# Performance work log

Measured on AMD Instinct MI355X. Metric: run time of the kernel, lower is better.

## Reference

```python
import jax, jax.numpy as jnp
import numpy as np

MODEL_DIM = 1024
NUM_HEADS = 16
HEAD_DIM = MODEL_DIM // NUM_HEADS


def setup_inputs() -> dict:
    key = jax.random.key(0)
    ks = jax.random.split(key, 9)
    s = 1.0 / np.sqrt(MODEL_DIM)
    d = {
        "query": jax.random.normal(ks[0], (2, 2048, MODEL_DIM), dtype=jnp.float32),
        "Wq": jax.random.normal(ks[1], (MODEL_DIM, MODEL_DIM), dtype=jnp.float32) * s,
        "bq": jnp.zeros((MODEL_DIM,), dtype=jnp.float32),
        "Wk": jax.random.normal(ks[2], (MODEL_DIM, MODEL_DIM), dtype=jnp.float32) * s,
        "bk": jnp.zeros((MODEL_DIM,), dtype=jnp.float32),
        "Wv": jax.random.normal(ks[3], (MODEL_DIM, MODEL_DIM), dtype=jnp.float32) * s,
        "bv": jnp.zeros((MODEL_DIM,), dtype=jnp.float32),
        "Wo": jax.random.normal(ks[4], (MODEL_DIM, MODEL_DIM), dtype=jnp.float32) * s,
        "bo": jnp.zeros((MODEL_DIM,), dtype=jnp.float32),
    }
    return d


def reference(query, Wq, bq, Wk, bk, Wv, bv, Wo, bo):
    B, S, D = query.shape
    H, hd = NUM_HEADS, HEAD_DIM
    # self-attention: key = value = query
    q = (query @ Wq.T + bq).reshape(B, S, H, hd).transpose(0, 2, 1, 3)  # [B,H,S,hd]
    k = (query @ Wk.T + bk).reshape(B, S, H, hd).transpose(0, 2, 1, 3)
    v = (query @ Wv.T + bv).reshape(B, S, H, hd).transpose(0, 2, 1, 3)
    scores = jnp.einsum("bhqd,bhkd->bhqk", q, k) / np.sqrt(hd)  # [B,H,S,S]
    attn = jax.nn.softmax(scores, axis=-1)
    ctx = jnp.einsum("bhqk,bhkd->bhqd", attn, v)  # [B,H,S,hd]
    ctx = ctx.transpose(0, 2, 1, 3).reshape(B, S, D)
    return ctx @ Wo.T + bo
```

## Files before the change

### kernel.cpp

```cpp
#include <hip/hip_runtime.h>

typedef __attribute__((ext_vector_type(8))) __bf16 bf16x8;
typedef __attribute__((ext_vector_type(8))) unsigned short ushort8;
typedef __attribute__((ext_vector_type(4))) unsigned short ushort4v;
typedef __attribute__((ext_vector_type(4))) float f32x4;
typedef __attribute__((ext_vector_type(2))) _Float16 f16x2;
typedef __attribute__((ext_vector_type(4))) _Float16 f16x4;
typedef __attribute__((ext_vector_type(8))) _Float16 f16x8;
typedef __attribute__((ext_vector_type(2))) __fp16 fp16v2;

__device__ __forceinline__ unsigned short f2bf(float f) {
    union { float f; unsigned int u; } c; c.f = f;
    unsigned int u = c.u;
    u += 0x7fffu + ((u >> 16) & 1u);
    return (unsigned short)(u >> 16);
}

__device__ __forceinline__ void async16(const void* g, void* l) {
    __builtin_amdgcn_global_load_lds(
        (const __attribute__((address_space(1))) unsigned int*)g,
        (__attribute__((address_space(3))) unsigned int*)l, 16, 0, 0);
}

__global__ __launch_bounds__(256) void cvt_all(
    const float* __restrict__ q,  const float* __restrict__ wq,
    const float* __restrict__ wk, const float* __restrict__ wv,
    const float* __restrict__ wo,
    unsigned short* __restrict__ q_bf, unsigned short* __restrict__ wqkv,
    unsigned short* __restrict__ wo_bf, float scale_k)
{
    const int NQ = 4096 * 1024, NW = 1024 * 1024;
    int i = (blockIdx.x * 256 + threadIdx.x) * 4;
    const float* src; unsigned short* dst; float sc = 1.0f; int off;
    if (i < NQ)               { src = q;  dst = q_bf;          off = i; }
    else if (i < NQ + NW)     { src = wq; dst = wqkv;          off = i - NQ; }
    else if (i < NQ + 2 * NW) { src = wk; dst = wqkv + NW;     off = i - NQ - NW; sc = scale_k; }
    else if (i < NQ + 3 * NW) { src = wv; dst = wqkv + 2 * NW; off = i - NQ - 2 * NW; }
    else                      { src = wo; dst = wo_bf;         off = i - NQ - 3 * NW; }
    float4 v = *(const float4*)(src + off);
    ushort4v o;
    o[0] = f2bf(v.x * sc); o[1] = f2bf(v.y * sc);
    o[2] = f2bf(v.z * sc); o[3] = f2bf(v.w * sc);
    *(ushort4v*)(dst + off) = o;
}

__global__ __launch_bounds__(256) void qkv_gemm(
    const unsigned short* __restrict__ A,
    const unsigned short* __restrict__ B,
    unsigned short* __restrict__ Cout,
    const float* __restrict__ b0, const float* __restrict__ b1, const float* __restrict__ b2,
    float s1)
{
    __shared__ __align__(16) unsigned short As[128 * 64];
    __shared__ __align__(16) unsigned short Bs[128 * 64];

    const int tid  = threadIdx.x;
    const int lane = tid & 63, wave = tid >> 6;
    const int quad = lane >> 4, l15 = lane & 15;
    const int wm = wave >> 1, wn = wave & 1;
    const int by = blockIdx.y, bx = blockIdx.x;
    const int K = 1024, N = 3072;

    const int srow = lane >> 3;
    const int sp   = lane & 7;
    const int scl  = sp ^ srow;
    const int sw   = l15 & 7;

    f32x4 acc[4][4];
#pragma unroll
    for (int i = 0; i < 4; ++i)
#pragma unroll
        for (int j = 0; j < 4; ++j) acc[i][j] = (f32x4)(0.0f);

    for (int kt = 0; kt < 16; ++kt) {
        __syncthreads();
#pragma unroll
        for (int j = 0; j < 4; ++j) {
            int r0 = wave * 32 + j * 8;
            async16(A + (size_t)(by * 128 + r0 + srow) * K + kt * 64 + scl * 8, &As[r0 * 64]);
            async16(B + (size_t)(bx * 128 + r0 + srow) * K + kt * 64 + scl * 8, &Bs[r0 * 64]);
        }
        __syncthreads();

#pragma unroll
        for (int kh = 0; kh < 2; ++kh) {
            bf16x8 af[4], bfr[4];
#pragma unroll
            for (int mi = 0; mi < 4; ++mi)
                af[mi] = __builtin_bit_cast(bf16x8,
                    *(const ushort8*)&As[(wm * 64 + mi * 16 + l15) * 64 + ((kh * 4 + quad) ^ sw) * 8]);
#pragma unroll
            for (int ni = 0; ni < 4; ++ni)
                bfr[ni] = __builtin_bit_cast(bf16x8,
                    *(const ushort8*)&Bs[(wn * 64 + ni * 16 + l15) * 64 + ((kh * 4 + quad) ^ sw) * 8]);
#pragma unroll
            for (int mi = 0; mi < 4; ++mi)
#pragma unroll
                for (int ni = 0; ni < 4; ++ni)
                    acc[mi][ni] = __builtin_amdgcn_mfma_f32_16x16x32_bf16(af[mi], bfr[ni], acc[mi][ni], 0, 0, 0);
        }
    }

#pragma unroll
    for (int ni = 0; ni < 4; ++ni) {
        int n = bx * 128 + wn * 64 + ni * 16 + l15;
        float bias = (n < 1024) ? b0[n] : (n < 2048 ? b1[n - 1024] * s1 : b2[n - 2048]);
#pragma unroll
        for (int mi = 0; mi < 4; ++mi) {
#pragma unroll
            for (int r = 0; r < 4; ++r) {
                int m = by * 128 + wm * 64 + mi * 16 + quad * 4 + r;
                Cout[(size_t)m * N + n] = f2bf(acc[mi][ni][r] + bias);
            }
        }
    }
}

__global__ __launch_bounds__(256) void out_gemm(
    const unsigned short* __restrict__ A,
    const unsigned short* __restrict__ B,
    float* __restrict__ Cout,
    const float* __restrict__ bo)
{
    __shared__ __align__(16) unsigned short As[128 * 64];
    __shared__ __align__(16) unsigned short Bs[64 * 64];

    const int tid  = threadIdx.x;
    const int lane = tid & 63, wave = tid >> 6;
    const int quad = lane >> 4, l15 = lane & 15;
    const int wm = wave >> 1, wn = wave & 1;
    const int by = blockIdx.y, bx = blockIdx.x;
    const int K = 1024;

    const int srow = lane >> 3;
    const int sp   = lane & 7;
    const int scl  = sp ^ srow;
    const int sw   = l15 & 7;

    f32x4 acc[4][2];
#pragma unroll
    for (int i = 0; i < 4; ++i)
#pragma unroll
        for (int j = 0; j < 2; ++j) acc[i][j] = (f32x4)(0.0f);

    for (int kt = 0; kt < 16; ++kt) {
        __syncthreads();
#pragma unroll
        for (int j = 0; j < 4; ++j) {
            int r0 = wave * 32 + j * 8;
            async16(A + (size_t)(by * 128 + r0 + srow) * K + kt * 64 + scl * 8, &As[r0 * 64]);
        }
#pragma unroll
        for (int j = 0; j < 2; ++j) {
            int r0 = wave * 16 + j * 8;
            async16(B + (size_t)(bx * 64 + r0 + srow) * K + kt * 64 + scl * 8, &Bs[r0 * 64]);
        }
        __syncthreads();

#pragma unroll
        for (int kh = 0; kh < 2; ++kh) {
            bf16x8 af[4], bfr[2];
#pragma unroll
            for (int mi = 0; mi < 4; ++mi)
                af[mi] = __builtin_bit_cast(bf16x8,
                    *(const ushort8*)&As[(wm * 64 + mi * 16 + l15) * 64 + ((kh * 4 + quad) ^ sw) * 8]);
#pragma unroll
            for (int ni = 0; ni < 2; ++ni)
                bfr[ni] = __builtin_bit_cast(bf16x8,
                    *(const ushort8*)&Bs[(wn * 32 + ni * 16 + l15) * 64 + ((kh * 4 + quad) ^ sw) * 8]);
#pragma unroll
            for (int mi = 0; mi < 4; ++mi)
#pragma unroll
                for (int ni = 0; ni < 2; ++ni)
                    acc[mi][ni] = __builtin_amdgcn_mfma_f32_16x16x32_bf16(af[mi], bfr[ni], acc[mi][ni], 0, 0, 0);
        }
    }

#pragma unroll
    for (int ni = 0; ni < 2; ++ni) {
        int n = bx * 64 + wn * 32 + ni * 16 + l15;
        float bias = bo[n];
#pragma unroll
        for (int mi = 0; mi < 4; ++mi) {
#pragma unroll
            for (int r = 0; r < 4; ++r) {
                int m = by * 128 + wm * 64 + mi * 16 + quad * 4 + r;
                Cout[(size_t)m * 1024 + n] = acc[mi][ni][r] + bias;
            }
        }
    }
}

__global__ __launch_bounds__(256) void transpose_v(const unsigned short* __restrict__ qkv,
                                                   _Float16* __restrict__ vtg)
{
    __shared__ unsigned short Ls[64][68];
    const int tid = threadIdx.x;
    const int bh = blockIdx.y, st = blockIdx.x;
    const int b = bh >> 4, h = bh & 15;

#pragma unroll
    for (int i = 0; i < 2; ++i) {
        int s = tid + i * 256;
        int row = s >> 3, c8 = (s & 7) << 3;
        ushort8 v = *(const ushort8*)(qkv + (size_t)(b * 2048 + st * 64 + row) * 3072 + 2048 + h * 64 + c8);
        *(ushort8*)&Ls[row][c8] = v;
    }
    __syncthreads();
#pragma unroll
    for (int i = 0; i < 2; ++i) {
        int s = tid + i * 256;
        int hd = s >> 3, p = s & 7;
        int cl = p ^ (hd & 7);
        int g = cl >> 2, q = cl & 3;
        f16x8 o;
#pragma unroll
        for (int e = 0; e < 8; ++e) {
            int kv = g * 32 + (e >> 2) * 16 + q * 4 + (e & 3);
            union { float f; unsigned int u; } c;
            c.u = ((unsigned int)Ls[kv][hd]) << 16;
            o[e] = (_Float16)c.f;
        }
        *(f16x8*)(vtg + (size_t)(bh * 64 + hd) * 2048 + st * 64 + p * 8) = o;
    }
}

__global__ __launch_bounds__(256) void attn(const unsigned short* __restrict__ qkv,
                                            const _Float16* __restrict__ vtg,
                                            unsigned short* __restrict__ ctx)
{
    __shared__ __align__(16) unsigned short Ks[64 * 64];
    __shared__ __align__(16) _Float16 Vt[64 * 64];

    const int tid  = threadIdx.x;
    const int lane = tid & 63, wave = tid >> 6;
    const int quad = lane >> 4, l15 = lane & 15;
    const int bh = blockIdx.y;
    const int b = bh >> 4, h = bh & 15;
    const int q0 = blockIdx.x * 128;

    const int srow = lane >> 3;
    const int sp   = lane & 7;
    const int scl  = sp ^ srow;
    const int sw   = l15 & 7;

    bf16x8 qf[2][2];
#pragma unroll
    for (int s = 0; s < 2; ++s) {
        int qrow = b * 2048 + q0 + wave * 32 + s * 16 + l15;
#pragma unroll
        for (int kh = 0; kh < 2; ++kh)
            qf[s][kh] = __builtin_bit_cast(bf16x8,
                *(const ushort8*)(qkv + (size_t)qrow * 3072 + h * 64 + kh * 32 + quad * 8));
    }

    f32x4 ot[2][4];
#pragma unroll
    for (int s = 0; s < 2; ++s)
#pragma unroll
        for (int ht = 0; ht < 4; ++ht) ot[s][ht] = (f32x4)(0.0f);
    float l_acc[2] = {0.0f, 0.0f};
    const fp16v2 ones = {(__fp16)1.0f, (__fp16)1.0f};

    for (int kt = 0; kt < 32; ++kt) {
        __syncthreads();
#pragma unroll
        for (int i = 0; i < 2; ++i) {
            int row = i * 32 + wave * 8 + srow;
            async16(qkv + (size_t)(b * 2048 + kt * 64 + row) * 3072 + 1024 + h * 64 + scl * 8,
                    &Ks[(i * 32 + wave * 8) * 64]);
            async16(vtg + (size_t)(bh * 64 + row) * 2048 + kt * 64 + sp * 8,
                    (unsigned short*)&Vt[(i * 32 + wave * 8) * 64]);
        }
        __syncthreads();

        f16x4 pv[2][4];
#pragma unroll
        for (int mt = 0; mt < 4; ++mt) {
            const unsigned short* kb = &Ks[(mt * 16 + l15) * 64];
            bf16x8 k0 = __builtin_bit_cast(bf16x8, *(const ushort8*)(kb + (quad ^ sw) * 8));
            bf16x8 k1 = __builtin_bit_cast(bf16x8, *(const ushort8*)(kb + ((quad ^ sw) ^ 4) * 8));
#pragma unroll
            for (int s = 0; s < 2; ++s) {
                f32x4 s4 = (f32x4)(0.0f);
                s4 = __builtin_amdgcn_mfma_f32_16x16x32_bf16(k0, qf[s][0], s4, 0, 0, 0);
                s4 = __builtin_amdgcn_mfma_f32_16x16x32_bf16(k1, qf[s][1], s4, 0, 0, 0);
                float p0 = __builtin_amdgcn_exp2f(s4[0]);
                float p1 = __builtin_amdgcn_exp2f(s4[1]);
                float p2 = __builtin_amdgcn_exp2f(s4[2]);
                float p3 = __builtin_amdgcn_exp2f(s4[3]);
                fp16v2 lo = __builtin_amdgcn_cvt_pkrtz(p0, p1);
                fp16v2 hi = __builtin_amdgcn_cvt_pkrtz(p2, p3);
                l_acc[s] = __builtin_amdgcn_fdot2(lo, ones, l_acc[s], false);
                l_acc[s] = __builtin_amdgcn_fdot2(hi, ones, l_acc[s], false);
                f16x2 lo2 = __builtin_bit_cast(f16x2, lo);
                f16x2 hi2 = __builtin_bit_cast(f16x2, hi);
                pv[s][mt] = __builtin_shufflevector(lo2, hi2, 0, 1, 2, 3);
            }
        }

#pragma unroll
        for (int ht = 0; ht < 4; ++ht) {
            const _Float16* vb = &Vt[(ht * 16 + l15) * 64];
#pragma unroll
            for (int g = 0; g < 2; ++g) {
                f16x8 v8 = *(const f16x8*)(vb + (((g * 4 + quad) ^ sw)) * 8);
                f16x4 vlo = __builtin_shufflevector(v8, v8, 0, 1, 2, 3);
                f16x4 vhi = __builtin_shufflevector(v8, v8, 4, 5, 6, 7);
#pragma unroll
                for (int s = 0; s < 2; ++s) {
                    ot[s][ht] = __builtin_amdgcn_mfma_f32_16x16x16f16(vlo, pv[s][2 * g],     ot[s][ht], 0, 0, 0);
                    ot[s][ht] = __builtin_amdgcn_mfma_f32_16x16x16f16(vhi, pv[s][2 * g + 1], ot[s][ht], 0, 0, 0);
                }
            }
        }
    }

#pragma unroll
    for (int s = 0; s < 2; ++s) {
        float l = l_acc[s];
        l += __shfl_xor(l, 16, 64);
        l += __shfl_xor(l, 32, 64);
        float inv = 1.0f / l;
        int qrow = b * 2048 + q0 + wave * 32 + s * 16 + l15;
#pragma unroll
        for (int ht = 0; ht < 4; ++ht) {
            ushort4v o4;
#pragma unroll
            for (int r = 0; r < 4; ++r) o4[r] = f2bf(ot[s][ht][r] * inv);
            *(ushort4v*)(ctx + (size_t)qrow * 1024 + h * 64 + ht * 16 + quad * 4) = o4;
        }
    }
}

extern "C" void kernel_launch(void* const* d_in, const int* in_sizes, int n_in,
                              void* d_out, int out_size, void* d_ws, size_t ws_size,
                              hipStream_t stream) {
    const float* query = (const float*)d_in[0];
    const float* Wq = (const float*)d_in[1];
    const float* bq = (const float*)d_in[2];
    const float* Wk = (const float*)d_in[3];
    const float* bk = (const float*)d_in[4];
    const float* Wv = (const float*)d_in[5];
    const float* bv = (const float*)d_in[6];
    const float* Wo = (const float*)d_in[7];
    const float* bo = (const float*)d_in[8];

    char* ws = (char*)d_ws;
    unsigned short* q_bf  = (unsigned short*)(ws);
    _Float16*       vtg   = (_Float16*)(ws);
    unsigned short* wqkv  = (unsigned short*)(ws + 8388608);
    unsigned short* wo_bf = (unsigned short*)(ws + 14680064);
    unsigned short* qkv   = (unsigned short*)(ws + 16777216);
    unsigned short* ctx   = (unsigned short*)(ws + 41943040);

    const float SCALE = 0.125f * 1.4426950408889634f;

    cvt_all<<<8192, 256, 0, stream>>>(query, Wq, Wk, Wv, Wo, q_bf, wqkv, wo_bf, SCALE);
    qkv_gemm<<<dim3(24, 32), 256, 0, stream>>>(q_bf, wqkv, qkv, bq, bk, bv, SCALE);
    transpose_v<<<dim3(32, 32), 256, 0, stream>>>(qkv, vtg);
    attn<<<dim3(16, 32), 256, 0, stream>>>(qkv, vtg, ctx);
    out_gemm<<<dim3(16, 32), 256, 0, stream>>>(ctx, wo_bf, (float*)d_out, bo);
}
```

Measured before the change: 202.9 us.

## Double-buffer LDS tiles in output GEMM and attention kernels

Splits the shared-memory tiles of the output projection GEMM and the attention kernel into two buffers. The next K/V or A/B tile is issued with async global-to-LDS loads while the current buffer is being computed, with two barriers per pair of iterations. This is meant to hide global load latency that was previously exposed between the load and compute barriers. In exchange it doubles LDS usage per block, which may lower occupancy. If the compiler inserts conservative vmcnt waits before the LDS reads, the overlap may be lost.

Result: slower. 207.7 us (+2.4%).

```diff
diff --git a/kernel.cpp b/kernel.cpp
--- a/kernel.cpp
+++ b/kernel.cpp
@@ -122,8 +122,8 @@
     float* __restrict__ Cout,
     const float* __restrict__ bo)
 {
-    __shared__ __align__(16) unsigned short As[128 * 64];
-    __shared__ __align__(16) unsigned short Bs[64 * 64];
+    __shared__ __align__(16) unsigned short As[2][128 * 64];
+    __shared__ __align__(16) unsigned short Bs[2][64 * 64];
 
     const int tid  = threadIdx.x;
     const int lane = tid & 63, wave = tid >> 6;
@@ -143,37 +143,47 @@
 #pragma unroll
         for (int j = 0; j < 2; ++j) acc[i][j] = (f32x4)(0.0f);
 
-    for (int kt = 0; kt < 16; ++kt) {
-        __syncthreads();
+    auto stage = [&](int kt, int p) {
 #pragma unroll
         for (int j = 0; j < 4; ++j) {
             int r0 = wave * 32 + j * 8;
-            async16(A + (size_t)(by * 128 + r0 + srow) * K + kt * 64 + scl * 8, &As[r0 * 64]);
+            async16(A + (size_t)(by * 128 + r0 + srow) * K + kt * 64 + scl * 8, &As[p][r0 * 64]);
         }
 #pragma unroll
         for (int j = 0; j < 2; ++j) {
             int r0 = wave * 16 + j * 8;
-            async16(B + (size_t)(bx * 64 + r0 + srow) * K + kt * 64 + scl * 8, &Bs[r0 * 64]);
-        }
-        __syncthreads();
-
+            async16(B + (size_t)(bx * 64 + r0 + srow) * K + kt * 64 + scl * 8, &Bs[p][r0 * 64]);
+        }
+    };
+
+    auto compute = [&](int p) {
 #pragma unroll
         for (int kh = 0; kh < 2; ++kh) {
             bf16x8 af[4], bfr[2];
 #pragma unroll
             for (int mi = 0; mi < 4; ++mi)
                 af[mi] = __builtin_bit_cast(bf16x8,
-                    *(const ushort8*)&As[(wm * 64 + mi * 16 + l15) * 64 + ((kh * 4 + quad) ^ sw) * 8]);
+                    *(const ushort8*)&As[p][(wm * 64 + mi * 16 + l15) * 64 + ((kh * 4 + quad) ^ sw) * 8]);
 #pragma unroll
             for (int ni = 0; ni < 2; ++ni)
                 bfr[ni] = __builtin_bit_cast(bf16x8,
-                    *(const ushort8*)&Bs[(wn * 32 + ni * 16 + l15) * 64 + ((kh * 4 + quad) ^ sw) * 8]);
+                    *(const ushort8*)&Bs[p][(wn * 32 + ni * 16 + l15) * 64 + ((kh * 4 + quad) ^ sw) * 8]);
 #pragma unroll
             for (int mi = 0; mi < 4; ++mi)
 #pragma unroll
                 for (int ni = 0; ni < 2; ++ni)
                     acc[mi][ni] = __builtin_amdgcn_mfma_f32_16x16x32_bf16(af[mi], bfr[ni], acc[mi][ni], 0, 0, 0);
         }
+    };
+
+    stage(0, 0);
+    for (int t = 0; t < 8; ++t) {
+        __syncthreads();
+        stage(2 * t + 1, 1);
+        compute(0);
+        __syncthreads();
+        if (t < 7) stage(2 * t + 2, 0);
+        compute(1);
     }
 
 #pragma unroll
@@ -229,8 +239,8 @@
                                             const _Float16* __restrict__ vtg,
                                             unsigned short* __restrict__ ctx)
 {
-    __shared__ __align__(16) unsigned short Ks[64 * 64];
-    __shared__ __align__(16) _Float16 Vt[64 * 64];
+    __shared__ __align__(16) unsigned short Ks[2][64 * 64];
+    __shared__ __align__(16) _Float16 Vt[2][64 * 64];
 
     const int tid  = threadIdx.x;
     const int lane = tid & 63, wave = tid >> 6;
@@ -244,6 +254,19 @@
     const int scl  = sp ^ srow;
     const int sw   = l15 & 7;
 
+    auto stage = [&](int kt, int p) {
+#pragma unroll
+        for (int i = 0; i < 2; ++i) {
+            int row = i * 32 + wave * 8 + srow;
+            async16(qkv + (size_t)(b * 2048 + kt * 64 + row) * 3072 + 1024 + h * 64 + scl * 8,
+                    &Ks[p][(i * 32 + wave * 8) * 64]);
+            async16(vtg + (size_t)(bh * 64 + row) * 2048 + kt * 64 + sp * 8,
+                    (unsigned short*)&Vt[p][(i * 32 + wave * 8) * 64]);
+        }
+    };
+
+    stage(0, 0);
+
     bf16x8 qf[2][2];
 #pragma unroll
     for (int s = 0; s < 2; ++s) {
@@ -262,22 +285,11 @@
     float l_acc[2] = {0.0f, 0.0f};
     const fp16v2 ones = {(__fp16)1.0f, (__fp16)1.0f};
 
-    for (int kt = 0; kt < 32; ++kt) {
-        __syncthreads();
-#pragma unroll
-        for (int i = 0; i < 2; ++i) {
-            int row = i * 32 + wave * 8 + srow;
-            async16(qkv + (size_t)(b * 2048 + kt * 64 + row) * 3072 + 1024 + h * 64 + scl * 8,
-                    &Ks[(i * 32 + wave * 8) * 64]);
-            async16(vtg + (size_t)(bh * 64 + row) * 2048 + kt * 64 + sp * 8,
-                    (unsigned short*)&Vt[(i * 32 + wave * 8) * 64]);
-        }
-        __syncthreads();
-
+    auto compute = [&](int p) {
         f16x4 pv[2][4];
 #pragma unroll
         for (int mt = 0; mt < 4; ++mt) {
-            const unsigned short* kb = &Ks[(mt * 16 + l15) * 64];
+            const unsigned short* kb = &Ks[p][(mt * 16 + l15) * 64];
             bf16x8 k0 = __builtin_bit_cast(bf16x8, *(const ushort8*)(kb + (quad ^ sw) * 8));
             bf16x8 k1 = __builtin_bit_cast(bf16x8, *(const ushort8*)(kb + ((quad ^ sw) ^ 4) * 8));
 #pragma unroll
@@ -301,7 +313,7 @@
 
 #pragma unroll
         for (int ht = 0; ht < 4; ++ht) {
-            const _Float16* vb = &Vt[(ht * 16 + l15) * 64];
+            const _Float16* vb = &Vt[p][(ht * 16 + l15) * 64];
 #pragma unroll
             for (int g = 0; g < 2; ++g) {
                 f16x8 v8 = *(const f16x8*)(vb + (((g * 4 + quad) ^ sw)) * 8);
@@ -314,6 +326,15 @@
                 }
             }
         }
+    };
+
+    for (int t = 0; t < 16; ++t) {
+        __syncthreads();
+        stage(2 * t + 1, 1);
+        compute(0);
+        __syncthreads();
+        if (t < 15) stage(2 * t + 2, 0);
+        compute(1);
     }
 
 #pragma unroll
```

## Fuse V transpose into QKV GEMM epilogue, drop transpose_v kernel

Applied to the files above, without the earlier changes.

The QKV GEMM epilogue now writes V tiles straight into the transposed, swizzled fp16 layout the attention kernel expects, and stores Q/K in a narrower 2048-wide buffer. The separate transpose_v kernel and its round trip of V through global memory are removed. The V stores are 8-byte scattered writes along head-dim rows, which may coalesce less well than the old row-major stores. The workspace layout is rearranged to match.

Result: faster. 195.8 us (median of 2 runs) (-3.5%).

```diff
diff --git a/kernel.cpp b/kernel.cpp
--- a/kernel.cpp
+++ b/kernel.cpp
@@ -47,7 +47,8 @@
 __global__ __launch_bounds__(256) void qkv_gemm(
     const unsigned short* __restrict__ A,
     const unsigned short* __restrict__ B,
-    unsigned short* __restrict__ Cout,
+    unsigned short* __restrict__ qkv,
+    _Float16* __restrict__ vtg,
     const float* __restrict__ b0, const float* __restrict__ b1, const float* __restrict__ b2,
     float s1)
 {
@@ -59,7 +60,7 @@
     const int quad = lane >> 4, l15 = lane & 15;
     const int wm = wave >> 1, wn = wave & 1;
     const int by = blockIdx.y, bx = blockIdx.x;
-    const int K = 1024, N = 3072;
+    const int K = 1024;
 
     const int srow = lane >> 3;
     const int sp   = lane & 7;
@@ -101,16 +102,37 @@
         }
     }
 
-#pragma unroll
-    for (int ni = 0; ni < 4; ++ni) {
-        int n = bx * 128 + wn * 64 + ni * 16 + l15;
-        float bias = (n < 1024) ? b0[n] : (n < 2048 ? b1[n - 1024] * s1 : b2[n - 2048]);
-#pragma unroll
-        for (int mi = 0; mi < 4; ++mi) {
-#pragma unroll
-            for (int r = 0; r < 4; ++r) {
-                int m = by * 128 + wm * 64 + mi * 16 + quad * 4 + r;
-                Cout[(size_t)m * N + n] = f2bf(acc[mi][ni][r] + bias);
+    if (bx < 16) {
+#pragma unroll
+        for (int ni = 0; ni < 4; ++ni) {
+            int n = bx * 128 + wn * 64 + ni * 16 + l15;
+            float bias = (n < 1024) ? b0[n] : b1[n - 1024] * s1;
+#pragma unroll
+            for (int mi = 0; mi < 4; ++mi) {
+#pragma unroll
+                for (int r = 0; r < 4; ++r) {
+                    int m = by * 128 + wm * 64 + mi * 16 + quad * 4 + r;
+                    qkv[(size_t)m * 2048 + n] = f2bf(acc[mi][ni][r] + bias);
+                }
+            }
+        }
+    } else {
+        const int mb = by * 128 + wm * 64;
+        const int b  = mb >> 11;
+        const int st = (mb & 2047) >> 6;
+#pragma unroll
+        for (int ni = 0; ni < 4; ++ni) {
+            int vf = (bx - 16) * 128 + wn * 64 + ni * 16 + l15;
+            int h = vf >> 6, hd = vf & 63;
+            float bias = b2[vf];
+            _Float16* vrow = vtg + ((size_t)((b * 16 + h) * 64 + hd)) * 2048 + st * 64;
+#pragma unroll
+            for (int mi = 0; mi < 4; ++mi) {
+                int p = ((mi >> 1) * 4 + quad) ^ (l15 & 7);
+                f16x4 o;
+#pragma unroll
+                for (int r = 0; r < 4; ++r) o[r] = (_Float16)(acc[mi][ni][r] + bias);
+                *(f16x4*)(vrow + p * 8 + (mi & 1) * 4) = o;
             }
         }
     }
@@ -191,40 +213,6 @@
     }
 }
 
-__global__ __launch_bounds__(256) void transpose_v(const unsigned short* __restrict__ qkv,
-                                                   _Float16* __restrict__ vtg)
-{
-    __shared__ unsigned short Ls[64][68];
-    const int tid = threadIdx.x;
-    const int bh = blockIdx.y, st = blockIdx.x;
-    const int b = bh >> 4, h = bh & 15;
-
-#pragma unroll
-    for (int i = 0; i < 2; ++i) {
-        int s = tid + i * 256;
-        int row = s >> 3, c8 = (s & 7) << 3;
-        ushort8 v = *(const ushort8*)(qkv + (size_t)(b * 2048 + st * 64 + row) * 3072 + 2048 + h * 64 + c8);
-        *(ushort8*)&Ls[row][c8] = v;
-    }
-    __syncthreads();
-#pragma unroll
-    for (int i = 0; i < 2; ++i) {
-        int s = tid + i * 256;
-        int hd = s >> 3, p = s & 7;
-        int cl = p ^ (hd & 7);
-        int g = cl >> 2, q = cl & 3;
-        f16x8 o;
-#pragma unroll
-        for (int e = 0; e < 8; ++e) {
-            int kv = g * 32 + (e >> 2) * 16 + q * 4 + (e & 3);
-            union { float f; unsigned int u; } c;
-            c.u = ((unsigned int)Ls[kv][hd]) << 16;
-            o[e] = (_Float16)c.f;
-        }
-        *(f16x8*)(vtg + (size_t)(bh * 64 + hd) * 2048 + st * 64 + p * 8) = o;
-    }
-}
-
 __global__ __launch_bounds__(256) void attn(const unsigned short* __restrict__ qkv,
                                             const _Float16* __restrict__ vtg,
                                             unsigned short* __restrict__ ctx)
@@ -251,7 +239,7 @@
 #pragma unroll
         for (int kh = 0; kh < 2; ++kh)
             qf[s][kh] = __builtin_bit_cast(bf16x8,
-                *(const ushort8*)(qkv + (size_t)qrow * 3072 + h * 64 + kh * 32 + quad * 8));
+                *(const ushort8*)(qkv + (size_t)qrow * 2048 + h * 64 + kh * 32 + quad * 8));
     }
 
     f32x4 ot[2][4];
@@ -267,7 +255,7 @@
 #pragma unroll
         for (int i = 0; i < 2; ++i) {
             int row = i * 32 + wave * 8 + srow;
-            async16(qkv + (size_t)(b * 2048 + kt * 64 + row) * 3072 + 1024 + h * 64 + scl * 8,
+            async16(qkv + (size_t)(b * 2048 + kt * 64 + row) * 2048 + 1024 + h * 64 + scl * 8,
                     &Ks[(i * 32 + wave * 8) * 64]);
             async16(vtg + (size_t)(bh * 64 + row) * 2048 + kt * 64 + sp * 8,
                     (unsigned short*)&Vt[(i * 32 + wave * 8) * 64]);
@@ -348,17 +336,16 @@
 
     char* ws = (char*)d_ws;
     unsigned short* q_bf  = (unsigned short*)(ws);
-    _Float16*       vtg   = (_Float16*)(ws);
+    unsigned short* ctx   = (unsigned short*)(ws);
     unsigned short* wqkv  = (unsigned short*)(ws + 8388608);
     unsigned short* wo_bf = (unsigned short*)(ws + 14680064);
     unsigned short* qkv   = (unsigned short*)(ws + 16777216);
-    unsigned short* ctx   = (unsigned short*)(ws + 41943040);
+    _Float16*       vtg   = (_Float16*)(ws + 33554432);
 
     const float SCALE = 0.125f * 1.4426950408889634f;
 
     cvt_all<<<8192, 256, 0, stream>>>(query, Wq, Wk, Wv, Wo, q_bf, wqkv, wo_bf, SCALE);
-    qkv_gemm<<<dim3(24, 32), 256, 0, stream>>>(q_bf, wqkv, qkv, bq, bk, bv, SCALE);
-    transpose_v<<<dim3(32, 32), 256, 0, stream>>>(qkv, vtg);
+    qkv_gemm<<<dim3(24, 32), 256, 0, stream>>>(q_bf, wqkv, qkv, vtg, bq, bk, bv, SCALE);
     attn<<<dim3(16, 32), 256, 0, stream>>>(qkv, vtg, ctx);
     out_gemm<<<dim3(16, 32), 256, 0, stream>>>(ctx, wo_bf, (float*)d_out, bo);
 }
```
